# Performance work log

Hardware: AMD Instinct MI355X
Metric: run time of the kernel (lower is better)

Reference implementation:

```python
import jax, jax.numpy as jnp
import numpy as np

D_MODEL = 1024
N_HEADS = 16
D_HEAD = D_MODEL // N_HEADS


def setup_inputs() -> dict:
    key = jax.random.key(0)
    ks = jax.random.split(key, 9)
    s = 1.0 / np.sqrt(D_MODEL)
    x = jax.random.normal(ks[0], (2, 2048, D_MODEL), dtype=jnp.float32)
    # torch nn.Linear stores weight [out, in]; we store [in, out] for x @ W
    Wq = jax.random.uniform(ks[1], (D_MODEL, D_MODEL), jnp.float32, -s, s)
    bq = jax.random.uniform(ks[2], (D_MODEL,), jnp.float32, -s, s)
    Wk = jax.random.uniform(ks[3], (D_MODEL, D_MODEL), jnp.float32, -s, s)
    bk = jax.random.uniform(ks[4], (D_MODEL,), jnp.float32, -s, s)
    Wv = jax.random.uniform(ks[5], (D_MODEL, D_MODEL), jnp.float32, -s, s)
    bv = jax.random.uniform(ks[6], (D_MODEL,), jnp.float32, -s, s)
    Wo = jax.random.uniform(ks[7], (D_MODEL, D_MODEL), jnp.float32, -s, s)
    bo = jax.random.uniform(ks[8], (D_MODEL,), jnp.float32, -s, s)
    return {"x": x, "Wq": Wq, "bq": bq, "Wk": Wk, "bk": bk,
            "Wv": Wv, "bv": bv, "Wo": Wo, "bo": bo}


def reference(x, Wq, bq, Wk, bk, Wv, bv, Wo, bo):
    B, S, _ = x.shape
    # project and split heads: [B, H, S, Dh]
    def split(t):
        return t.reshape(B, S, N_HEADS, D_HEAD).transpose(0, 2, 1, 3)
    Q = split(x @ Wq + bq)
    K = split(x @ Wk + bk)
    V = split(x @ Wv + bv)
    scale = 1.0 / jnp.sqrt(jnp.asarray(D_HEAD, x.dtype))
    scores = jnp.einsum('bhqd,bhkd->bhqk', Q, K) * scale  # [B,H,S,S]
    attn = jax.nn.softmax(scores, axis=-1)
    out = jnp.einsum('bhqk,bhkd->bhqd', attn, V)  # [B,H,S,Dh]
    out = out.transpose(0, 2, 1, 3).reshape(B, S, D_MODEL)
    return out @ Wo + bo
```

## Files before the change

### kernel.cpp

```cpp
#include <hip/hip_runtime.h>
#include <hip/hip_bf16.h>
#include <cmath>

#define D_MODEL 1024
#define N_HEADS 16
#define D_HEAD  64
#define BATCH   2
#define SEQ     2048
#define M_TOT   (BATCH*SEQ)
#define NELT    ((size_t)M_TOT * D_MODEL)

typedef __attribute__((ext_vector_type(8))) short short8;
typedef __attribute__((ext_vector_type(4))) float f32x4;

#define QSCALE (0.125f * 1.44269504088896f)

static __device__ __forceinline__ ushort f2bf(float f) {
    __hip_bfloat16 h = __float2bfloat16(f);
    return *reinterpret_cast<ushort*>(&h);
}

static __device__ __forceinline__ float exp2_raw(float x) {
    return __builtin_amdgcn_exp2f(x);
}

static __device__ __forceinline__ void gload_lds16(const void* g, void* l) {
    __builtin_amdgcn_global_load_lds((const __attribute__((address_space(1))) unsigned*)g,
                                     (__attribute__((address_space(3))) unsigned*)l,
                                     16, 0, 0);
}

__global__ __launch_bounds__(256)
void prep_kernel(const float* __restrict__ x,
                 const float* __restrict__ W0, const float* __restrict__ W1,
                 const float* __restrict__ W2, const float* __restrict__ W3,
                 ushort* __restrict__ xb, ushort* __restrict__ Wt0)
{
    __shared__ float Ts[64][65];
    const int z = blockIdx.z;
    const int t = threadIdx.x;

    if (z == 4) {
        const int slab = blockIdx.y * 16 + blockIdx.x;
#pragma unroll
        for (int u = 0; u < 16; ++u) {
            const int i = slab * 4096 + u * 256 + t;
            const float4 v = ((const float4*)x)[i];
            ushort4 uo;
            uo.x = f2bf(v.x); uo.y = f2bf(v.y); uo.z = f2bf(v.z); uo.w = f2bf(v.w);
            ((ushort4*)xb)[i] = uo;
        }
        return;
    }

    const float* W = (z == 0) ? W0 : (z == 1) ? W1 : (z == 2) ? W2 : W3;
    ushort* Wt = Wt0 + (size_t)z * D_MODEL * D_MODEL;

    const int n0 = blockIdx.x * 64;
    const int k0 = blockIdx.y * 64;
    const int rr = t >> 4;
    const int c4 = (t & 15) * 4;

#pragma unroll
    for (int i = 0; i < 4; ++i) {
        const int r = rr + i * 16;
        const float4 v = *(const float4*)&W[(size_t)(k0 + r) * D_MODEL + n0 + c4];
        Ts[r][c4 + 0] = v.x; Ts[r][c4 + 1] = v.y;
        Ts[r][c4 + 2] = v.z; Ts[r][c4 + 3] = v.w;
    }
    __syncthreads();
#pragma unroll
    for (int i = 0; i < 4; ++i) {
        const int nn = rr + i * 16;
        ushort4 u;
        u.x = f2bf(Ts[c4 + 0][nn]); u.y = f2bf(Ts[c4 + 1][nn]);
        u.z = f2bf(Ts[c4 + 2][nn]); u.w = f2bf(Ts[c4 + 3][nn]);
        *(ushort4*)&Wt[(size_t)(n0 + nn) * D_MODEL + k0 + c4] = u;
    }
}

__global__ __launch_bounds__(256)
void gemm_qkv_mfma(const ushort* __restrict__ A, const ushort* __restrict__ Bt,
                   const float* __restrict__ bq, const float* __restrict__ bk,
                   const float* __restrict__ bv, ushort* __restrict__ QKV)
{
    __shared__ ushort SH[128 * 136];
    ushort* As = SH;
    ushort* Bs = SH + 128 * 64;

    const int t    = threadIdx.x;
    const int lane = t & 63;
    const int w    = t >> 6;
    const int wr   = w >> 1;
    const int wc   = w & 1;
    const int l16  = lane & 15;
    const int g    = lane >> 4;
    const int m0   = blockIdx.y * 128;
    const int n0   = blockIdx.x * 128;

    f32x4 acc[4][4];
#pragma unroll
    for (int i = 0; i < 4; ++i)
#pragma unroll
        for (int j = 0; j < 4; ++j) acc[i][j] = f32x4{0.f, 0.f, 0.f, 0.f};

    for (int kt = 0; kt < D_MODEL; kt += 64) {
        __syncthreads();
        const ushort* Ag = A  + (size_t)m0 * D_MODEL + kt;
        const ushort* Bg = Bt + (size_t)n0 * D_MODEL + kt;
#pragma unroll
        for (int it = 0; it < 4; ++it) {
            const int b   = (it * 256 + t) * 16;
            const int row = b >> 7;
            const int src = (b & 127) ^ ((row & 7) << 4);
            const int lof = (it * 256 + (t & ~63)) * 8;
            gload_lds16(Ag + (size_t)row * D_MODEL + (src >> 1), As + lof);
            gload_lds16(Bg + (size_t)row * D_MODEL + (src >> 1), Bs + lof);
        }
        __syncthreads();

#pragma unroll
        for (int kh = 0; kh < 2; ++kh) {
            short8 a[4], bfr[4];
#pragma unroll
            for (int fm = 0; fm < 4; ++fm) {
                const int row  = wr * 64 + fm * 16 + l16;
                const int byte = row * 128 + (((kh << 6) | (g << 4)) ^ ((row & 7) << 4));
                a[fm] = *(const short8*)((const char*)As + byte);
            }
#pragma unroll
            for (int fn = 0; fn < 4; ++fn) {
                const int row  = wc * 64 + fn * 16 + l16;
                const int byte = row * 128 + (((kh << 6) | (g << 4)) ^ ((row & 7) << 4));
                bfr[fn] = *(const short8*)((const char*)Bs + byte);
            }
#pragma unroll
            for (int fm = 0; fm < 4; ++fm)
#pragma unroll
                for (int fn = 0; fn < 4; ++fn)
                    acc[fm][fn] = __builtin_amdgcn_mfma_f32_16x16x32_bf16(a[fm], bfr[fn], acc[fm][fn], 0, 0, 0);
        }
    }

    const int proj = n0 >> 10;

    if (proj == 2) {
        __syncthreads();
#pragma unroll
        for (int fm = 0; fm < 4; ++fm) {
            const int ml = wr * 64 + fm * 16 + g * 4;
#pragma unroll
            for (int fn = 0; fn < 4; ++fn) {
                const int nnl = wc * 64 + fn * 16 + l16;
                const float bn = bv[(n0 & 1023) + nnl];
                ushort4 pk;
                pk.x = f2bf(acc[fm][fn][0] + bn);
                pk.y = f2bf(acc[fm][fn][1] + bn);
                pk.z = f2bf(acc[fm][fn][2] + bn);
                pk.w = f2bf(acc[fm][fn][3] + bn);
                *(ushort4*)((char*)SH + nnl * 256 + ((ml * 2) ^ ((nnl & 15) << 4))) = pk;
            }
        }
        __syncthreads();
        const int bb  = m0 >> 11;
        const int sA0 = m0 & (SEQ - 1);
        const int ch  = t & 15;
#pragma unroll
        for (int pass = 0; pass < 8; ++pass) {
            const int rr = pass * 16 + (t >> 4);
            const int nn = (n0 & 1023) + rr;
            const int h  = nn >> 6;
            const int dh = nn & 63;
            const short8 v = *(const short8*)((const char*)SH + rr * 256 +
                                              ((ch * 16) ^ ((rr & 15) << 4)));
            *(short8*)&QKV[2 * NELT + (((size_t)(bb * N_HEADS + h)) * D_HEAD + dh) * SEQ
                           + sA0 + ch * 8] = v;
        }
        return;
    }

    __syncthreads();
    const float sc = (proj == 0) ? QSCALE : 1.0f;
#pragma unroll
    for (int fm = 0; fm < 4; ++fm) {
        const int mlb = wr * 64 + fm * 16 + g * 4;
#pragma unroll
        for (int fn = 0; fn < 4; ++fn) {
            const int nnl = wc * 64 + fn * 16 + l16;
            const float bn = (proj == 0) ? bq[(n0 & 1023) + nnl] : bk[(n0 & 1023) + nnl];
#pragma unroll
            for (int r = 0; r < 4; ++r)
                SH[(mlb + r) * 136 + nnl] = f2bf((acc[fm][fn][r] + bn) * sc);
        }
    }
    __syncthreads();
    {
        ushort* outp = QKV + (size_t)proj * NELT;
        const int bb  = m0 >> 11;
        const int sA0 = m0 & (SEQ - 1);
        const int ch  = t & 15;
#pragma unroll
        for (int pass = 0; pass < 8; ++pass) {
            const int rr = pass * 16 + (t >> 4);
            const int nn = (n0 & 1023) + ch * 8;
            const int h  = nn >> 6;
            const int dh = nn & 63;
            const short8 v = *(const short8*)&SH[rr * 136 + ch * 8];
            *(short8*)&outp[(((size_t)(bb * N_HEADS + h)) * SEQ + sA0 + rr) * D_HEAD + dh] = v;
        }
    }
}

__global__ __launch_bounds__(256)
void gemm_out_mfma(const ushort* __restrict__ A, const ushort* __restrict__ Bt,
                   const float* __restrict__ bias, float* __restrict__ outp)
{
    __shared__ ushort As[64 * 64];
    __shared__ ushort Bs[128 * 64];

    const int t    = threadIdx.x;
    const int lane = t & 63;
    const int w    = t >> 6;
    const int l16  = lane & 15;
    const int g    = lane >> 4;
    const int m0   = blockIdx.y * 64;
    const int n0   = blockIdx.x * 128;

    f32x4 acc[4][2];
#pragma unroll
    for (int i = 0; i < 4; ++i)
#pragma unroll
        for (int j = 0; j < 2; ++j) acc[i][j] = f32x4{0.f, 0.f, 0.f, 0.f};

    for (int kt = 0; kt < D_MODEL; kt += 64) {
        __syncthreads();
        const ushort* Ag = A  + (size_t)m0 * D_MODEL + kt;
        const ushort* Bg = Bt + (size_t)n0 * D_MODEL + kt;
#pragma unroll
        for (int it = 0; it < 2; ++it) {
            const int b   = (it * 256 + t) * 16;
            const int row = b >> 7;
            const int src = (b & 127) ^ ((row & 7) << 4);
            const int lof = (it * 256 + (t & ~63)) * 8;
            gload_lds16(Ag + (size_t)row * D_MODEL + (src >> 1), As + lof);
        }
#pragma unroll
        for (int it = 0; it < 4; ++it) {
            const int b   = (it * 256 + t) * 16;
            const int row = b >> 7;
            const int src = (b & 127) ^ ((row & 7) << 4);
            const int lof = (it * 256 + (t & ~63)) * 8;
            gload_lds16(Bg + (size_t)row * D_MODEL + (src >> 1), Bs + lof);
        }
        __syncthreads();

#pragma unroll
        for (int kh = 0; kh < 2; ++kh) {
            short8 a[4], bfr[2];
#pragma unroll
            for (int fm = 0; fm < 4; ++fm) {
                const int row  = fm * 16 + l16;
                const int byte = row * 128 + (((kh << 6) | (g << 4)) ^ ((row & 7) << 4));
                a[fm] = *(const short8*)((const char*)As + byte);
            }
#pragma unroll
            for (int fn = 0; fn < 2; ++fn) {
                const int row  = w * 32 + fn * 16 + l16;
                const int byte = row * 128 + (((kh << 6) | (g << 4)) ^ ((row & 7) << 4));
                bfr[fn] = *(const short8*)((const char*)Bs + byte);
            }
#pragma unroll
            for (int fm = 0; fm < 4; ++fm)
#pragma unroll
                for (int fn = 0; fn < 2; ++fn)
                    acc[fm][fn] = __builtin_amdgcn_mfma_f32_16x16x32_bf16(a[fm], bfr[fn], acc[fm][fn], 0, 0, 0);
        }
    }

#pragma unroll
    for (int fm = 0; fm < 4; ++fm) {
        const int mb = m0 + fm * 16 + g * 4;
#pragma unroll
        for (int fn = 0; fn < 2; ++fn) {
            const int n  = n0 + w * 32 + fn * 16 + l16;
            const float bn = bias[n];
#pragma unroll
            for (int r = 0; r < 4; ++r)
                outp[(size_t)(mb + r) * D_MODEL + n] = acc[fm][fn][r] + bn;
        }
    }
}

__global__ __launch_bounds__(256)
void flash_attn_mfma(const ushort* __restrict__ Q, const ushort* __restrict__ K,
                     const ushort* __restrict__ Vt, ushort* __restrict__ AO)
{
    __shared__ ushort Kl[2][128 * 64];
    __shared__ ushort Vl[2][64 * 128];
    __shared__ ushort Ps[4][16 * 64];

    const int t    = threadIdx.x;
    const int w    = t >> 6;
    const int lane = t & 63;
    const int l16  = lane & 15;
    const int g    = lane >> 4;
    const int i    = blockIdx.x;
    const int slot = i >> 3;
    const int bh   = (i & 7) * 4 + (slot >> 4);
    const int qt   = slot & 15;

    const size_t qkbase = (size_t)bh * SEQ * D_HEAD;
    const ushort* Vg0 = Vt + (size_t)bh * D_HEAD * SEQ;

    short8 qf[2][2];
#pragma unroll
    for (int tt = 0; tt < 2; ++tt) {
        const int q0 = qt * 128 + w * 32 + tt * 16;
        const ushort* qp = Q + qkbase + (size_t)(q0 + l16) * D_HEAD + g * 8;
        qf[tt][0] = *(const short8*)(qp);
        qf[tt][1] = *(const short8*)(qp + 32);
    }

    f32x4 o[2][4];
    float m_r[2], l_r[2];
#pragma unroll
    for (int tt = 0; tt < 2; ++tt) {
        m_r[tt] = -INFINITY; l_r[tt] = 0.f;
#pragma unroll
        for (int d = 0; d < 4; ++d) o[tt][d] = f32x4{0.f, 0.f, 0.f, 0.f};
    }

    auto stage = [&](int ktile, int b) {
        const ushort* Kg = K + qkbase + (size_t)(ktile * 128) * D_HEAD;
        const ushort* Vg = Vg0 + ktile * 128;
#pragma unroll
        for (int it = 0; it < 4; ++it) {
            const int bb   = (it * 256 + t) * 16;
            const int lof  = (it * 256 + (t & ~63)) * 8;
            const int rowK = bb >> 7;
            const int srcK = (bb & 127) ^ ((rowK & 7) << 4);
            gload_lds16(Kg + (size_t)rowK * D_HEAD + (srcK >> 1), &Kl[b][lof]);
            const int rowV = bb >> 8;
            const int srcV = (bb & 255) ^ ((rowV & 15) << 4);
            gload_lds16(Vg + (size_t)rowV * SEQ + (srcV >> 1), &Vl[b][lof]);
        }
    };

    stage(0, 0);
    __syncthreads();

    const int NT = SEQ / 128;
    for (int kt = 0; kt < NT; ++kt) {
        const int buf = kt & 1;
        if (kt + 1 < NT) stage(kt + 1, buf ^ 1);

#pragma unroll
        for (int h2 = 0; h2 < 2; ++h2) {
            short8 kf[4][2];
#pragma unroll
            for (int nt = 0; nt < 4; ++nt) {
                const int row = h2 * 64 + nt * 16 + l16;
#pragma unroll
                for (int ks = 0; ks < 2; ++ks) {
                    const int byte = row * 128 + (((ks * 64) | (g * 16)) ^ ((row & 7) << 4));
                    kf[nt][ks] = *(const short8*)((const char*)&Kl[buf][0] + byte);
                }
            }

            short8 vf[4][2];
#pragma unroll
            for (int dt = 0; dt < 4; ++dt) {
                const int row = dt * 16 + l16;
#pragma unroll
                for (int ks = 0; ks < 2; ++ks) {
                    const int byte = row * 256 + ((h2 * 128 + ks * 64 + g * 16) ^ ((row & 15) << 4));
                    vf[dt][ks] = *(const short8*)((const char*)&Vl[buf][0] + byte);
                }
            }

            f32x4 st[2][4];
#pragma unroll
            for (int tt = 0; tt < 2; ++tt)
#pragma unroll
                for (int nt = 0; nt < 4; ++nt) {
                    f32x4 a = f32x4{0.f, 0.f, 0.f, 0.f};
                    a = __builtin_amdgcn_mfma_f32_16x16x32_bf16(kf[nt][0], qf[tt][0], a, 0, 0, 0);
                    a = __builtin_amdgcn_mfma_f32_16x16x32_bf16(kf[nt][1], qf[tt][1], a, 0, 0, 0);
                    st[tt][nt] = a;
                }

#pragma unroll
            for (int tt = 0; tt < 2; ++tt) {
                float pmax = st[tt][0][0];
#pragma unroll
                for (int nt = 0; nt < 4; ++nt)
#pragma unroll
                    for (int r = 0; r < 4; ++r) pmax = fmaxf(pmax, st[tt][nt][r]);
                pmax = fmaxf(pmax, __shfl_xor(pmax, 16, 64));
                pmax = fmaxf(pmax, __shfl_xor(pmax, 32, 64));

                if (__any(pmax - m_r[tt] > 8.f)) {
                    const float mnew  = fmaxf(m_r[tt], pmax);
                    const float alpha = exp2_raw(m_r[tt] - mnew);
                    m_r[tt] = mnew;
                    l_r[tt] *= alpha;
                    float ar[4];
#pragma unroll
                    for (int r = 0; r < 4; ++r) ar[r] = __shfl(alpha, g * 4 + r, 64);
#pragma unroll
                    for (int dt = 0; dt < 4; ++dt)
#pragma unroll
                        for (int r = 0; r < 4; ++r) o[tt][dt][r] *= ar[r];
                }

                float rs = 0.f;
#pragma unroll
                for (int nt = 0; nt < 4; ++nt) {
                    ushort4 pk;
#pragma unroll
                    for (int r = 0; r < 4; ++r) {
                        const float p = exp2_raw(st[tt][nt][r] - m_r[tt]);
                        rs += p;
                        ((ushort*)&pk)[r] = f2bf(p);
                    }
                    const int pb = (nt * 32 + g * 8) ^ ((l16 & 7) << 4);
                    *(ushort4*)((char*)&Ps[w][0] + l16 * 128 + pb) = pk;
                }
                rs += __shfl_xor(rs, 16, 64);
                rs += __shfl_xor(rs, 32, 64);
                l_r[tt] += rs;

#pragma unroll
                for (int ks = 0; ks < 2; ++ks) {
                    const int rb = (ks * 64 + g * 16) ^ ((l16 & 7) << 4);
                    const short8 pf = *(const short8*)((const char*)&Ps[w][0] + l16 * 128 + rb);
#pragma unroll
                    for (int dt = 0; dt < 4; ++dt)
                        o[tt][dt] = __builtin_amdgcn_mfma_f32_16x16x32_bf16(pf, vf[dt][ks], o[tt][dt], 0, 0, 0);
                }
            }
        }

        __syncthreads();
    }

    const int b = bh >> 4;
    const int h = bh & 15;
#pragma unroll
    for (int tt = 0; tt < 2; ++tt) {
        const int q0 = qt * 128 + w * 32 + tt * 16;
        float lr_row[4];
#pragma unroll
        for (int r = 0; r < 4; ++r) lr_row[r] = __shfl(l_r[tt], g * 4 + r, 64);
#pragma unroll
        for (int r = 0; r < 4; ++r) {
            const float inv = 1.f / lr_row[r];
            const size_t row = (size_t)b * SEQ + q0 + g * 4 + r;
#pragma unroll
            for (int dt = 0; dt < 4; ++dt)
                AO[row * D_MODEL + h * D_HEAD + dt * 16 + l16] = f2bf(o[tt][dt][r] * inv);
        }
    }
}

extern "C" void kernel_launch(void* const* d_in, const int* in_sizes, int n_in,
                              void* d_out, int out_size, void* d_ws, size_t ws_size,
                              hipStream_t stream)
{
    const float* x  = (const float*)d_in[0];
    const float* Wq = (const float*)d_in[1];
    const float* bq = (const float*)d_in[2];
    const float* Wk = (const float*)d_in[3];
    const float* bk = (const float*)d_in[4];
    const float* Wv = (const float*)d_in[5];
    const float* bv = (const float*)d_in[6];
    const float* Wo = (const float*)d_in[7];
    const float* bo = (const float*)d_in[8];
    float* out = (float*)d_out;

    const size_t WELT = (size_t)D_MODEL * D_MODEL;
    ushort* xb  = (ushort*)d_ws;
    ushort* Wqt = xb + NELT;
    ushort* Wot = Wqt + 3 * WELT;
    ushort* Qb  = xb + 2 * NELT;
    ushort* Kb  = Qb + NELT;
    ushort* Vtb = Kb + NELT;
    ushort* AOb = xb + 5 * NELT;

    prep_kernel<<<dim3(D_MODEL / 64, D_MODEL / 64, 5), 256, 0, stream>>>(x, Wq, Wk, Wv, Wo, xb, Wqt);
    gemm_qkv_mfma<<<dim3(3 * D_MODEL / 128, M_TOT / 128), 256, 0, stream>>>(xb, Wqt, bq, bk, bv, Qb);
    flash_attn_mfma<<<dim3(512), 256, 0, stream>>>(Qb, Kb, Vtb, AOb);
    gemm_out_mfma<<<dim3(D_MODEL / 128, M_TOT / 64), 256, 0, stream>>>(AOb, Wot, bo, out);
}
```

Measured before the change: 125.1 us.

## Halve flash-attention query and key tiles to double block count

The attention kernel now handles a 64-query tile per block (one 16-row tile per wave) and streams 64-key tiles instead of 128. The launch grows from 512 to 1024 blocks, and each block needs half the LDS and fewer registers, so more blocks can be resident per CU. The row-sum shuffle reduction moves out of the inner loop and runs once at the end. In exchange, each K/V tile loaded into LDS is reused by half as many queries, and there are twice as many loop iterations with a block barrier each.

```diff
diff --git a/kernel.cpp b/kernel.cpp
--- a/kernel.cpp
+++ b/kernel.cpp
@@ -283,7 +283,7 @@
 #pragma unroll
         for (int fn = 0; fn < 2; ++fn) {
             const int n  = n0 + w * 32 + fn * 16 + l16;
-            const float bn = bias[n];
+            const float bn = bias[fn * 16 + l16 + n0 + w * 32];
 #pragma unroll
             for (int r = 0; r < 4; ++r)
                 outp[(size_t)(mb + r) * D_MODEL + n] = acc[fm][fn][r] + bn;
@@ -295,8 +295,8 @@
 void flash_attn_mfma(const ushort* __restrict__ Q, const ushort* __restrict__ K,
                      const ushort* __restrict__ Vt, ushort* __restrict__ AO)
 {
-    __shared__ ushort Kl[2][128 * 64];
-    __shared__ ushort Vl[2][64 * 128];
+    __shared__ ushort Kl[2][64 * 64];
+    __shared__ ushort Vl[2][64 * 64];
     __shared__ ushort Ps[4][16 * 64];
 
     const int t    = threadIdx.x;
@@ -306,160 +306,142 @@
     const int g    = lane >> 4;
     const int i    = blockIdx.x;
     const int slot = i >> 3;
-    const int bh   = (i & 7) * 4 + (slot >> 4);
-    const int qt   = slot & 15;
-
+    const int bh   = (i & 7) * 4 + (slot >> 5);
+    const int qt   = slot & 31;
+
+    const int q0 = qt * 64 + w * 16;
     const size_t qkbase = (size_t)bh * SEQ * D_HEAD;
     const ushort* Vg0 = Vt + (size_t)bh * D_HEAD * SEQ;
 
-    short8 qf[2][2];
-#pragma unroll
-    for (int tt = 0; tt < 2; ++tt) {
-        const int q0 = qt * 128 + w * 32 + tt * 16;
+    short8 qf[2];
+    {
         const ushort* qp = Q + qkbase + (size_t)(q0 + l16) * D_HEAD + g * 8;
-        qf[tt][0] = *(const short8*)(qp);
-        qf[tt][1] = *(const short8*)(qp + 32);
-    }
-
-    f32x4 o[2][4];
-    float m_r[2], l_r[2];
-#pragma unroll
-    for (int tt = 0; tt < 2; ++tt) {
-        m_r[tt] = -INFINITY; l_r[tt] = 0.f;
-#pragma unroll
-        for (int d = 0; d < 4; ++d) o[tt][d] = f32x4{0.f, 0.f, 0.f, 0.f};
-    }
+        qf[0] = *(const short8*)(qp);
+        qf[1] = *(const short8*)(qp + 32);
+    }
+
+    f32x4 o[4];
+    float m_r = -INFINITY, l_r = 0.f;
+#pragma unroll
+    for (int d = 0; d < 4; ++d) o[d] = f32x4{0.f, 0.f, 0.f, 0.f};
 
     auto stage = [&](int ktile, int b) {
-        const ushort* Kg = K + qkbase + (size_t)(ktile * 128) * D_HEAD;
-        const ushort* Vg = Vg0 + ktile * 128;
-#pragma unroll
-        for (int it = 0; it < 4; ++it) {
-            const int bb   = (it * 256 + t) * 16;
-            const int lof  = (it * 256 + (t & ~63)) * 8;
-            const int rowK = bb >> 7;
-            const int srcK = (bb & 127) ^ ((rowK & 7) << 4);
-            gload_lds16(Kg + (size_t)rowK * D_HEAD + (srcK >> 1), &Kl[b][lof]);
-            const int rowV = bb >> 8;
-            const int srcV = (bb & 255) ^ ((rowV & 15) << 4);
-            gload_lds16(Vg + (size_t)rowV * SEQ + (srcV >> 1), &Vl[b][lof]);
+        const ushort* Kg = K + qkbase + (size_t)(ktile * 64) * D_HEAD;
+        const ushort* Vg = Vg0 + ktile * 64;
+#pragma unroll
+        for (int it = 0; it < 2; ++it) {
+            const int bb  = (it * 256 + t) * 16;
+            const int row = bb >> 7;
+            const int src = (bb & 127) ^ ((row & 7) << 4);
+            const int lof = (it * 256 + (t & ~63)) * 8;
+            gload_lds16(Kg + (size_t)row * D_HEAD + (src >> 1), &Kl[b][lof]);
+            gload_lds16(Vg + (size_t)row * SEQ + (src >> 1), &Vl[b][lof]);
         }
     };
 
     stage(0, 0);
     __syncthreads();
 
-    const int NT = SEQ / 128;
+    const int NT = SEQ / 64;
     for (int kt = 0; kt < NT; ++kt) {
         const int buf = kt & 1;
         if (kt + 1 < NT) stage(kt + 1, buf ^ 1);
 
-#pragma unroll
-        for (int h2 = 0; h2 < 2; ++h2) {
-            short8 kf[4][2];
-#pragma unroll
-            for (int nt = 0; nt < 4; ++nt) {
-                const int row = h2 * 64 + nt * 16 + l16;
-#pragma unroll
-                for (int ks = 0; ks < 2; ++ks) {
-                    const int byte = row * 128 + (((ks * 64) | (g * 16)) ^ ((row & 7) << 4));
-                    kf[nt][ks] = *(const short8*)((const char*)&Kl[buf][0] + byte);
-                }
-            }
-
-            short8 vf[4][2];
-#pragma unroll
-            for (int dt = 0; dt < 4; ++dt) {
-                const int row = dt * 16 + l16;
-#pragma unroll
-                for (int ks = 0; ks < 2; ++ks) {
-                    const int byte = row * 256 + ((h2 * 128 + ks * 64 + g * 16) ^ ((row & 15) << 4));
-                    vf[dt][ks] = *(const short8*)((const char*)&Vl[buf][0] + byte);
-                }
-            }
-
-            f32x4 st[2][4];
-#pragma unroll
-            for (int tt = 0; tt < 2; ++tt)
-#pragma unroll
-                for (int nt = 0; nt < 4; ++nt) {
-                    f32x4 a = f32x4{0.f, 0.f, 0.f, 0.f};
-                    a = __builtin_amdgcn_mfma_f32_16x16x32_bf16(kf[nt][0], qf[tt][0], a, 0, 0, 0);
-                    a = __builtin_amdgcn_mfma_f32_16x16x32_bf16(kf[nt][1], qf[tt][1], a, 0, 0, 0);
-                    st[tt][nt] = a;
-                }
-
-#pragma unroll
-            for (int tt = 0; tt < 2; ++tt) {
-                float pmax = st[tt][0][0];
-#pragma unroll
-                for (int nt = 0; nt < 4; ++nt)
-#pragma unroll
-                    for (int r = 0; r < 4; ++r) pmax = fmaxf(pmax, st[tt][nt][r]);
-                pmax = fmaxf(pmax, __shfl_xor(pmax, 16, 64));
-                pmax = fmaxf(pmax, __shfl_xor(pmax, 32, 64));
-
-                if (__any(pmax - m_r[tt] > 8.f)) {
-                    const float mnew  = fmaxf(m_r[tt], pmax);
-                    const float alpha = exp2_raw(m_r[tt] - mnew);
-                    m_r[tt] = mnew;
-                    l_r[tt] *= alpha;
-                    float ar[4];
-#pragma unroll
-                    for (int r = 0; r < 4; ++r) ar[r] = __shfl(alpha, g * 4 + r, 64);
-#pragma unroll
-                    for (int dt = 0; dt < 4; ++dt)
-#pragma unroll
-                        for (int r = 0; r < 4; ++r) o[tt][dt][r] *= ar[r];
-                }
-
-                float rs = 0.f;
-#pragma unroll
-                for (int nt = 0; nt < 4; ++nt) {
-                    ushort4 pk;
-#pragma unroll
-                    for (int r = 0; r < 4; ++r) {
-                        const float p = exp2_raw(st[tt][nt][r] - m_r[tt]);
-                        rs += p;
-                        ((ushort*)&pk)[r] = f2bf(p);
-                    }
-                    const int pb = (nt * 32 + g * 8) ^ ((l16 & 7) << 4);
-                    *(ushort4*)((char*)&Ps[w][0] + l16 * 128 + pb) = pk;
-                }
-                rs += __shfl_xor(rs, 16, 64);
-                rs += __shfl_xor(rs, 32, 64);
-                l_r[tt] += rs;
-
-#pragma unroll
-                for (int ks = 0; ks < 2; ++ks) {
-                    const int rb = (ks * 64 + g * 16) ^ ((l16 & 7) << 4);
-                    const short8 pf = *(const short8*)((const char*)&Ps[w][0] + l16 * 128 + rb);
-#pragma unroll
-                    for (int dt = 0; dt < 4; ++dt)
-                        o[tt][dt] = __builtin_amdgcn_mfma_f32_16x16x32_bf16(pf, vf[dt][ks], o[tt][dt], 0, 0, 0);
-                }
-            }
-        }
-
-        __syncthreads();
-    }
+        short8 kf[4][2];
+#pragma unroll
+        for (int nt = 0; nt < 4; ++nt) {
+            const int row = nt * 16 + l16;
+#pragma unroll
+            for (int ks = 0; ks < 2; ++ks) {
+                const int byte = row * 128 + (((ks * 64) | (g * 16)) ^ ((row & 7) << 4));
+                kf[nt][ks] = *(const short8*)((const char*)&Kl[buf][0] + byte);
+            }
+        }
+        short8 vf[4][2];
+#pragma unroll
+        for (int dt = 0; dt < 4; ++dt) {
+            const int row = dt * 16 + l16;
+#pragma unroll
+            for (int ks = 0; ks < 2; ++ks) {
+                const int byte = row * 128 + (((ks * 64) | (g * 16)) ^ ((row & 7) << 4));
+                vf[dt][ks] = *(const short8*)((const char*)&Vl[buf][0] + byte);
+            }
+        }
+
+        f32x4 st[4];
+#pragma unroll
+        for (int nt = 0; nt < 4; ++nt) {
+            f32x4 a = f32x4{0.f, 0.f, 0.f, 0.f};
+            a = __builtin_amdgcn_mfma_f32_16x16x32_bf16(kf[nt][0], qf[0], a, 0, 0, 0);
+            a = __builtin_amdgcn_mfma_f32_16x16x32_bf16(kf[nt][1], qf[1], a, 0, 0, 0);
+            st[nt] = a;
+        }
+
+        float pmax = st[0][0];
+#pragma unroll
+        for (int nt = 0; nt < 4; ++nt)
+#pragma unroll
+            for (int r = 0; r < 4; ++r) pmax = fmaxf(pmax, st[nt][r]);
+        pmax = fmaxf(pmax, __shfl_xor(pmax, 16, 64));
+        pmax = fmaxf(pmax, __shfl_xor(pmax, 32, 64));
+
+        if (__any(pmax - m_r > 8.f)) {
+            const float mnew  = fmaxf(m_r, pmax);
+            const float alpha = exp2_raw(m_r - mnew);
+            m_r = mnew;
+            l_r *= alpha;
+            float ar[4];
+#pragma unroll
+            for (int r = 0; r < 4; ++r) ar[r] = __shfl(alpha, g * 4 + r, 64);
+#pragma unroll
+            for (int dt = 0; dt < 4; ++dt)
+#pragma unroll
+                for (int r = 0; r < 4; ++r) o[dt][r] *= ar[r];
+        }
+
+        float rs = 0.f;
+#pragma unroll
+        for (int nt = 0; nt < 4; ++nt) {
+            ushort4 pk;
+#pragma unroll
+            for (int r = 0; r < 4; ++r) {
+                const float p = exp2_raw(st[nt][r] - m_r);
+                rs += p;
+                ((ushort*)&pk)[r] = f2bf(p);
+            }
+            const int pb = (nt * 32 + g * 8) ^ ((l16 & 7) << 4);
+            *(ushort4*)((char*)&Ps[w][0] + l16 * 128 + pb) = pk;
+        }
+        l_r += rs;
+
+#pragma unroll
+        for (int ks = 0; ks < 2; ++ks) {
+            const int rb = (ks * 64 + g * 16) ^ ((l16 & 7) << 4);
+            const short8 pf = *(const short8*)((const char*)&Ps[w][0] + l16 * 128 + rb);
+#pragma unroll
+            for (int dt = 0; dt < 4; ++dt)
+                o[dt] = __builtin_amdgcn_mfma_f32_16x16x32_bf16(pf, vf[dt][ks], o[dt], 0, 0, 0);
+        }
+
+        __syncthreads();
+    }
+
+    float lt = l_r;
+    lt += __shfl_xor(lt, 16, 64);
+    lt += __shfl_xor(lt, 32, 64);
+    float lr_row[4];
+#pragma unroll
+    for (int r = 0; r < 4; ++r) lr_row[r] = __shfl(lt, g * 4 + r, 64);
 
     const int b = bh >> 4;
     const int h = bh & 15;
 #pragma unroll
-    for (int tt = 0; tt < 2; ++tt) {
-        const int q0 = qt * 128 + w * 32 + tt * 16;
-        float lr_row[4];
-#pragma unroll
-        for (int r = 0; r < 4; ++r) lr_row[r] = __shfl(l_r[tt], g * 4 + r, 64);
-#pragma unroll
-        for (int r = 0; r < 4; ++r) {
-            const float inv = 1.f / lr_row[r];
-            const size_t row = (size_t)b * SEQ + q0 + g * 4 + r;
-#pragma unroll
-            for (int dt = 0; dt < 4; ++dt)
-                AO[row * D_MODEL + h * D_HEAD + dt * 16 + l16] = f2bf(o[tt][dt][r] * inv);
-        }
+    for (int r = 0; r < 4; ++r) {
+        const float inv = 1.f / lr_row[r];
+        const size_t row = (size_t)b * SEQ + q0 + g * 4 + r;
+#pragma unroll
+        for (int dt = 0; dt < 4; ++dt)
+            AO[row * D_MODEL + h * D_HEAD + dt * 16 + l16] = f2bf(o[dt][r] * inv);
     }
 }
 
@@ -489,6 +471,6 @@
 
     prep_kernel<<<dim3(D_MODEL / 64, D_MODEL / 64, 5), 256, 0, stream>>>(x, Wq, Wk, Wv, Wo, xb, Wqt);
     gemm_qkv_mfma<<<dim3(3 * D_MODEL / 128, M_TOT / 128), 256, 0, stream>>>(xb, Wqt, bq, bk, bv, Qb);
-    flash_attn_mfma<<<dim3(512), 256, 0, stream>>>(Qb, Kb, Vtb, AOb);
+    flash_attn_mfma<<<dim3(1024), 256, 0, stream>>>(Qb, Kb, Vtb, AOb);
     gemm_out_mfma<<<dim3(D_MODEL / 128, M_TOT / 64), 256, 0, stream>>>(AOb, Wot, bo, out);
 }
```

New measurement: 133.5 us. 6.7% more time.
